# Kernel tuning notes

Hardware: AMD Instinct MI355X
Metric: run time of the kernel (lower is better)

The kernel has to match this reference:

```python
import jax, jax.numpy as jnp
import numpy as np

N_USERS = 100000
N_ITEMS = 50000
N_FACTORS = 64
N_LAYERS = 3
NNZ = 4800000


def setup_inputs() -> dict:
    key = jax.random.key(0)
    k1, k2, k3, k4, k5 = jax.random.split(key, 5)
    N = N_USERS + N_ITEMS
    return {
        "user_emb": 0.1 * jax.random.normal(k1, (N_USERS, N_FACTORS), dtype=jnp.float32),
        "item_emb": 0.1 * jax.random.normal(k2, (N_ITEMS, N_FACTORS), dtype=jnp.float32),
        "adj_row": jax.random.randint(k3, (NNZ,), 0, N, dtype=jnp.int32),
        "adj_col": jax.random.randint(k4, (NNZ,), 0, N, dtype=jnp.int32),
        "adj_val": jax.random.uniform(k5, (NNZ,), dtype=jnp.float32),
    }


def reference(user_emb, item_emb, adj_row, adj_col, adj_val):
    n_users = user_emb.shape[0]
    n_items = item_emb.shape[0]
    N = n_users + n_items

    # initial embeddings: concat users then items  [N, d]
    emb = jnp.concatenate([user_emb, item_emb], axis=0)

    def spmm(x):
        # sparse (COO) @ dense: gather source rows, scale, scatter-add to dest rows
        msgs = adj_val[:, None] * x[adj_col]          # [nnz, d]
        return jax.ops.segment_sum(msgs, adj_row, num_segments=N)

    # running mean over layer outputs (fuses stack+mean; dropout=0, eval mode)
    acc = emb
    for _ in range(N_LAYERS):
        emb = spmm(emb)
        acc = acc + emb
    mean_emb = acc / (N_LAYERS + 1)

    return mean_emb[:n_users], mean_emb[n_users:]
```

## Files before the change

### kernel.cpp

```cpp
#include <hip/hip_runtime.h>

static constexpr int D        = 64;
static constexpr int N_LAYERS = 3;
static constexpr int SH2      = 8;
static constexpr int T1       = 4096;
static constexpr int CAP      = 8896;
static constexpr int NINIT    = 448;


__device__ inline unsigned pack_bf2(float a, float b) {
    unsigned ua = __float_as_uint(a); ua = (ua + 0x7FFFu + ((ua >> 16) & 1u)) >> 16;
    unsigned ub = __float_as_uint(b); ub = (ub + 0x7FFFu + ((ub >> 16) & 1u)) >> 16;
    return ua | (ub << 16);
}
__device__ inline float blo(unsigned u) { return __uint_as_float(u << 16); }
__device__ inline float bhi(unsigned u) { return __uint_as_float(u & 0xFFFF0000u); }

__global__ __launch_bounds__(256) void k_part1f(const int* __restrict__ row,
                                                const int* __restrict__ col,
                                                const float* __restrict__ val,
                                                int* __restrict__ gcnt,
                                                unsigned* __restrict__ g1,
                                                unsigned char* __restrict__ lr,
                                                int nnz, int NB2, int nInit,
                                                const float4* __restrict__ ue,
                                                const float4* __restrict__ ie,
                                                uint4* __restrict__ cur,
                                                int nUser8, int nTot8) {
    __shared__ unsigned       sg1[T1];
    __shared__ unsigned char  slr[T1];
    __shared__ unsigned short bbin[T1];
    __shared__ unsigned short perm[T1];
    __shared__ int hist[768];
    __shared__ int binstart[768];
    __shared__ int gcur[768];
    __shared__ int bincur[768];
    __shared__ int wtot[4];

    int tid = threadIdx.x;
    int bid = blockIdx.x;
    int tile;
    if (bid < 2 * nInit) {
        if (bid & 1) {
            int stride = nInit * 256;
            for (int i = (bid >> 1) * 256 + tid; i < nTot8; i += stride) {
                float4 f0, f1;
                if (i < nUser8) { f0 = ue[2 * i];              f1 = ue[2 * i + 1]; }
                else            { int j = i - nUser8; f0 = ie[2 * j]; f1 = ie[2 * j + 1]; }
                cur[i] = make_uint4(pack_bf2(f0.x, f0.y), pack_bf2(f0.z, f0.w),
                                    pack_bf2(f1.x, f1.y), pack_bf2(f1.z, f1.w));
            }
            return;
        }
        tile = bid >> 1;
    } else {
        tile = bid - nInit;
    }

    int base = tile * T1;
    int n    = nnz - base; if (n > T1) n = T1;

    for (int b = tid; b < NB2; b += 256) { hist[b] = 0; bincur[b] = 0; }
    __syncthreads();

    for (int i = tid; i < n; i += 256) {
        int e = base + i;
        int r = row[e];
        int q = (int)(val[e] * 16384.f + 0.5f);
        if (q > 16383) q = 16383;
        sg1[i]  = ((unsigned)col[e] << 14) | (unsigned)q;
        slr[i]  = (unsigned char)(r & ((1 << SH2) - 1));
        int b   = r >> SH2;
        bbin[i] = (unsigned short)b;
        atomicAdd(&hist[b], 1);
    }
    __syncthreads();

    int per = (NB2 + 255) / 256;
    int i0  = tid * per;
    int sum = 0;
    for (int k = 0; k < per; ++k) { int i = i0 + k; if (i < NB2) sum += hist[i]; }
    int inc = sum;
    #pragma unroll
    for (int o = 1; o < 64; o <<= 1) {
        int t = __shfl_up(inc, o);
        if ((tid & 63) >= o) inc += t;
    }
    if ((tid & 63) == 63) wtot[tid >> 6] = inc;
    __syncthreads();
    int wbase = 0;
    int w = tid >> 6;
    #pragma unroll
    for (int j = 0; j < 3; ++j) if (w > j) wbase += wtot[j];
    int run = wbase + inc - sum;
    for (int k = 0; k < per; ++k) {
        int i = i0 + k;
        if (i < NB2) { binstart[i] = run; run += hist[i]; }
    }
    __syncthreads();

    for (int b = tid; b < NB2; b += 256) {
        int c = hist[b];
        if (c) {
            int o = atomicAdd(&gcnt[b], c);
            int lim = CAP - c;
            if (o > lim) o = lim;
            gcur[b] = b * CAP + o;
        }
    }
    __syncthreads();

    for (int i = tid; i < n; i += 256) {
        int b = bbin[i];
        int rnk = binstart[b] + atomicAdd(&bincur[b], 1);
        perm[rnk] = (unsigned short)i;
    }
    __syncthreads();

    for (int j = tid; j < n; j += 256) {
        int i = perm[j];
        int b = bbin[i];
        int pos = gcur[b] + (j - binstart[b]);
        g1[pos] = sg1[i];
        lr[pos] = slr[i];
    }
}

__global__ __launch_bounds__(512) void k_part2(const int* __restrict__ gcnt,
                                               const unsigned* __restrict__ g1,
                                               const unsigned char* __restrict__ lr,
                                               unsigned* __restrict__ ecv,
                                               int2* __restrict__ rowptr2) {
    __shared__ int hist[256];
    __shared__ int cur[256];
    __shared__ int ssum[256];
    int b   = blockIdx.x;
    int tid = threadIdx.x;
    int lo  = b * CAP;
    int cnt = gcnt[b];
    if (cnt > CAP) cnt = CAP;

    if (tid < 256) hist[tid] = 0;
    __syncthreads();
    for (int i = tid; i < cnt; i += 512)
        atomicAdd(&hist[lr[lo + i]], 1);
    __syncthreads();

    if (tid < 256) ssum[tid] = hist[tid];
    __syncthreads();
    for (int off = 1; off < 256; off <<= 1) {
        int v = 0;
        if (tid < 256 && tid >= off) v = ssum[tid - off];
        __syncthreads();
        if (tid < 256) ssum[tid] += v;
        __syncthreads();
    }
    if (tid < 256) {
        int h    = hist[tid];
        int excl = ssum[tid] - h;
        cur[tid] = excl;
        rowptr2[(b << SH2) + tid] = make_int2(lo + excl, lo + excl + h);
    }
    __syncthreads();

    for (int i = tid; i < cnt; i += 512) {
        int r = lr[lo + i];
        int p = atomicAdd(&cur[r], 1);
        ecv[lo + p] = g1[lo + i];
    }
}

template <bool LAST>
__global__ void k_spmm_bf(const int2* __restrict__ rowptr2,
                          const unsigned* __restrict__ ecv,
                          const uint4* __restrict__ x, uint4* __restrict__ y,
                          float* __restrict__ acc,
                          const uint4* __restrict__ e0b,
                          const uint4* __restrict__ y1,
                          int N) {
    int wid = (blockIdx.x * blockDim.x + threadIdx.x) >> 6;
    if (wid >= N) return;
    int lane = threadIdx.x & 63;
    int grp  = lane >> 3;
    unsigned ch = (unsigned)(lane & 7);
    int2 rp = rowptr2[wid];
    int e0 = rp.x;
    int e1 = rp.y;
    float s0 = 0.f, s1 = 0.f, s2 = 0.f, s3 = 0.f;
    float s4 = 0.f, s5 = 0.f, s6 = 0.f, s7 = 0.f;
    int e = e0 + grp;
    for (; e + 24 < e1; e += 32) {
        unsigned A0 = ecv[e];
        unsigned A1 = ecv[e + 8];
        unsigned A2 = ecv[e + 16];
        unsigned A3 = ecv[e + 24];
        uint4 x0 = x[((A0 >> 11) & ~7u) | ch];
        uint4 x1 = x[((A1 >> 11) & ~7u) | ch];
        uint4 x2 = x[((A2 >> 11) & ~7u) | ch];
        uint4 x3 = x[((A3 >> 11) & ~7u) | ch];
        float v0 = (float)(A0 & 0x3FFFu);
        float v1 = (float)(A1 & 0x3FFFu);
        float v2 = (float)(A2 & 0x3FFFu);
        float v3 = (float)(A3 & 0x3FFFu);
        s0 += v0 * blo(x0.x) + v1 * blo(x1.x) + v2 * blo(x2.x) + v3 * blo(x3.x);
        s1 += v0 * bhi(x0.x) + v1 * bhi(x1.x) + v2 * bhi(x2.x) + v3 * bhi(x3.x);
        s2 += v0 * blo(x0.y) + v1 * blo(x1.y) + v2 * blo(x2.y) + v3 * blo(x3.y);
        s3 += v0 * bhi(x0.y) + v1 * bhi(x1.y) + v2 * bhi(x2.y) + v3 * bhi(x3.y);
        s4 += v0 * blo(x0.z) + v1 * blo(x1.z) + v2 * blo(x2.z) + v3 * blo(x3.z);
        s5 += v0 * bhi(x0.z) + v1 * bhi(x1.z) + v2 * bhi(x2.z) + v3 * bhi(x3.z);
        s6 += v0 * blo(x0.w) + v1 * blo(x1.w) + v2 * blo(x2.w) + v3 * blo(x3.w);
        s7 += v0 * bhi(x0.w) + v1 * bhi(x1.w) + v2 * bhi(x2.w) + v3 * bhi(x3.w);
    }
    for (; e + 8 < e1; e += 16) {
        unsigned A = ecv[e];
        unsigned C = ecv[e + 8];
        uint4 xa = x[((A >> 11) & ~7u) | ch];
        uint4 xc = x[((C >> 11) & ~7u) | ch];
        float va = (float)(A & 0x3FFFu);
        float vc = (float)(C & 0x3FFFu);
        s0 += va * blo(xa.x) + vc * blo(xc.x);
        s1 += va * bhi(xa.x) + vc * bhi(xc.x);
        s2 += va * blo(xa.y) + vc * blo(xc.y);
        s3 += va * bhi(xa.y) + vc * bhi(xc.y);
        s4 += va * blo(xa.z) + vc * blo(xc.z);
        s5 += va * bhi(xa.z) + vc * bhi(xc.z);
        s6 += va * blo(xa.w) + vc * blo(xc.w);
        s7 += va * bhi(xa.w) + vc * bhi(xc.w);
    }
    if (e < e1) {
        unsigned A = ecv[e];
        uint4 xa = x[((A >> 11) & ~7u) | ch];
        float va = (float)(A & 0x3FFFu);
        s0 += va * blo(xa.x); s1 += va * bhi(xa.x);
        s2 += va * blo(xa.y); s3 += va * bhi(xa.y);
        s4 += va * blo(xa.z); s5 += va * bhi(xa.z);
        s6 += va * blo(xa.w); s7 += va * bhi(xa.w);
    }
    #pragma unroll
    for (int m = 8; m <= 32; m <<= 1) {
        s0 += __shfl_xor(s0, m); s1 += __shfl_xor(s1, m);
        s2 += __shfl_xor(s2, m); s3 += __shfl_xor(s3, m);
        s4 += __shfl_xor(s4, m); s5 += __shfl_xor(s5, m);
        s6 += __shfl_xor(s6, m); s7 += __shfl_xor(s7, m);
    }
    if (grp == 0) {
        if (!LAST) {
            const float SC = 1.f / 16384.f;
            y[(size_t)wid * 8 + ch] =
                make_uint4(pack_bf2(s0 * SC, s1 * SC), pack_bf2(s2 * SC, s3 * SC),
                           pack_bf2(s4 * SC, s5 * SC), pack_bf2(s6 * SC, s7 * SC));
        } else {
            const float SC25 = 0.25f / 16384.f;
            size_t ro = (size_t)wid * 8 + ch;
            uint4 u0 = e0b[ro];
            uint4 u1 = y1[ro];
            uint4 u2 = x [ro];
            float4 a0, a1;
            a0.x = (blo(u0.x) + blo(u1.x) + blo(u2.x)) * 0.25f + s0 * SC25;
            a0.y = (bhi(u0.x) + bhi(u1.x) + bhi(u2.x)) * 0.25f + s1 * SC25;
            a0.z = (blo(u0.y) + blo(u1.y) + blo(u2.y)) * 0.25f + s2 * SC25;
            a0.w = (bhi(u0.y) + bhi(u1.y) + bhi(u2.y)) * 0.25f + s3 * SC25;
            a1.x = (blo(u0.z) + blo(u1.z) + blo(u2.z)) * 0.25f + s4 * SC25;
            a1.y = (bhi(u0.z) + bhi(u1.z) + bhi(u2.z)) * 0.25f + s5 * SC25;
            a1.z = (blo(u0.w) + blo(u1.w) + blo(u2.w)) * 0.25f + s6 * SC25;
            a1.w = (bhi(u0.w) + bhi(u1.w) + bhi(u2.w)) * 0.25f + s7 * SC25;
            size_t o = ((size_t)wid << 6) + (ch << 3);
            *(float4*)(acc + o)     = a0;
            *(float4*)(acc + o + 4) = a1;
        }
    }
}

__global__ void k_init(const float4* __restrict__ ue, const float4* __restrict__ ie,
                       float4* __restrict__ cur, float4* __restrict__ acc,
                       int nUser4, int nTot4) {
    int stride = gridDim.x * blockDim.x;
    for (int i = blockIdx.x * blockDim.x + threadIdx.x; i < nTot4; i += stride) {
        float4 v = (i < nUser4) ? ue[i] : ie[i - nUser4];
        cur[i] = v;
        acc[i] = v;
    }
}

__global__ void k_spmm_atomic(const int* __restrict__ row, const int* __restrict__ col,
                              const float* __restrict__ val, const float* __restrict__ x,
                              float* __restrict__ y, int nnz) {
    long long total  = (long long)nnz * 16;
    long long stride = (long long)gridDim.x * blockDim.x;
    for (long long idx = (long long)blockIdx.x * blockDim.x + threadIdx.x;
         idx < total; idx += stride) {
        int e = (int)(idx >> 4);
        int c = (int)(idx & 15);
        int r = row[e];
        int ssrc = col[e];
        float v = val[e];
        float4 xv = *(const float4*)(x + (size_t)ssrc * D + c * 4);
        float* yp = y + (size_t)r * D + c * 4;
        atomicAdd(yp + 0, v * xv.x);
        atomicAdd(yp + 1, v * xv.y);
        atomicAdd(yp + 2, v * xv.z);
        atomicAdd(yp + 3, v * xv.w);
    }
}

__global__ void k_acc(const float4* __restrict__ nxt, float4* __restrict__ acc,
                      float scale, int n4) {
    int stride = gridDim.x * blockDim.x;
    for (int i = blockIdx.x * blockDim.x + threadIdx.x; i < n4; i += stride) {
        float4 a = acc[i];
        float4 b = nxt[i];
        a.x = (a.x + b.x) * scale;
        a.y = (a.y + b.y) * scale;
        a.z = (a.z + b.z) * scale;
        a.w = (a.w + b.w) * scale;
        acc[i] = a;
    }
}

extern "C" void kernel_launch(void* const* d_in, const int* in_sizes, int n_in,
                              void* d_out, int out_size, void* d_ws, size_t ws_size,
                              hipStream_t stream) {
    const float* ue  = (const float*)d_in[0];
    const float* ie  = (const float*)d_in[1];
    const int*   row = (const int*)  d_in[2];
    const int*   col = (const int*)  d_in[3];
    const float* val = (const float*)d_in[4];

    const int n_users = in_sizes[0] / D;
    const int n_items = in_sizes[1] / D;
    const int nnz     = in_sizes[2];
    const int N       = n_users + n_items;
    const int NB2     = (N + (1 << SH2) - 1) >> SH2;

    float* acc = (float*)d_out;
    const size_t bf16B = (size_t)N * D * 2;
    auto aup = [](size_t x) { return (x + 255) & ~(size_t)255; };

    size_t off = 0;
    uint4* buf0 = (uint4*)((char*)d_ws + off); off += aup(bf16B);
    uint4* buf1 = (uint4*)((char*)d_ws + off); off += aup(bf16B);
    uint4* buf2 = (uint4*)((char*)d_ws + off); off += aup(bf16B);
    unsigned*      g1 = (unsigned*)     ((char*)d_ws + off); off += aup((size_t)NB2 * CAP * 4);
    unsigned char* lr = (unsigned char*)((char*)d_ws + off); off += aup((size_t)NB2 * CAP);
    unsigned*      ecv = (unsigned*)    ((char*)d_ws + off); off += aup((size_t)NB2 * CAP * 4);
    int2* rowptr2 = (int2*)((char*)d_ws + off); off += aup((size_t)(NB2 << SH2) * 8);
    int*  gcnt    = (int*) ((char*)d_ws + off); off += aup((size_t)NB2 * 4);
    const size_t needCSR = off;

    bool capOK = ((size_t)nnz / NB2 + 600) <= (size_t)CAP && NB2 <= 768 &&
                 N <= (1 << 18);

    if (ws_size >= needCSR && capOK) {
        hipMemsetAsync(gcnt, 0, (size_t)NB2 * 4, stream);
        int nTiles = (nnz + T1 - 1) / T1;
        int nInit  = NINIT < nTiles ? NINIT : nTiles;
        int nTot8  = N * 8;
        int nUser8 = n_users * 8;
        k_part1f<<<nTiles + nInit, 256, 0, stream>>>(row, col, val, gcnt, g1, lr,
                                                     nnz, NB2, nInit,
                                                     (const float4*)ue, (const float4*)ie,
                                                     buf0, nUser8, nTot8);
        k_part2<<<NB2, 512, 0, stream>>>(gcnt, g1, lr, ecv, rowptr2);

        int grid = (N + 3) / 4;
        k_spmm_bf<false><<<grid, 256, 0, stream>>>(rowptr2, ecv, buf0, buf1,
                                                   nullptr, nullptr, nullptr, N);
        k_spmm_bf<false><<<grid, 256, 0, stream>>>(rowptr2, ecv, buf1, buf2,
                                                   nullptr, nullptr, nullptr, N);
        k_spmm_bf<true ><<<grid, 256, 0, stream>>>(rowptr2, ecv, buf2, nullptr,
                                                   acc, buf0, buf1, N);
    } else {
        const size_t denseB = (size_t)N * D * sizeof(float);
        float* fa = (float*)d_ws;
        float* fb = fa + (size_t)N * D;
        const int nTot4  = N * D / 4;
        const int nUser4 = n_users * D / 4;
        k_init<<<2048, 256, 0, stream>>>((const float4*)ue, (const float4*)ie,
                                         (float4*)fa, (float4*)acc, nUser4, nTot4);
        float* curp = fa;
        float* nxt  = fb;
        for (int l = 0; l < N_LAYERS; ++l) {
            hipMemsetAsync(nxt, 0, denseB, stream);
            k_spmm_atomic<<<8192, 256, 0, stream>>>(row, col, val, curp, nxt, nnz);
            float scale = (l == N_LAYERS - 1) ? (1.0f / (N_LAYERS + 1)) : 1.0f;
            k_acc<<<2048, 256, 0, stream>>>((const float4*)nxt, (float4*)acc, scale, nTot4);
            float* t = curp; curp = nxt; nxt = t;
        }
    }
}
```

Baseline: 470.5 us.

## Split CSR bucket build into histogram kernel and 4-way scatter kernel

The per-bucket CSR build kernel is split in two. The first computes row histograms and prefix offsets and writes per-row cursors to global memory. The second scatters edges using global atomics on those cursors, with four blocks per bucket. This raises parallelism beyond NB2 (~586) blocks, at the cost of an extra launch, global atomics instead of shared-memory ones, and a second read of lr.

```diff
diff --git a/kernel.cpp b/kernel.cpp
--- a/kernel.cpp
+++ b/kernel.cpp
@@ -126,13 +126,11 @@
     }
 }
 
-__global__ __launch_bounds__(512) void k_part2(const int* __restrict__ gcnt,
-                                               const unsigned* __restrict__ g1,
-                                               const unsigned char* __restrict__ lr,
-                                               unsigned* __restrict__ ecv,
-                                               int2* __restrict__ rowptr2) {
+__global__ __launch_bounds__(256) void k_part2a(const int* __restrict__ gcnt,
+                                                const unsigned char* __restrict__ lr,
+                                                int2* __restrict__ rowptr2,
+                                                int* __restrict__ grcur) {
     __shared__ int hist[256];
-    __shared__ int cur[256];
     __shared__ int ssum[256];
     int b   = blockIdx.x;
     int tid = threadIdx.x;
@@ -140,33 +138,42 @@
     int cnt = gcnt[b];
     if (cnt > CAP) cnt = CAP;
 
-    if (tid < 256) hist[tid] = 0;
-    __syncthreads();
-    for (int i = tid; i < cnt; i += 512)
+    hist[tid] = 0;
+    __syncthreads();
+    for (int i = tid; i < cnt; i += 256)
         atomicAdd(&hist[lr[lo + i]], 1);
     __syncthreads();
 
-    if (tid < 256) ssum[tid] = hist[tid];
+    int h = hist[tid];
+    ssum[tid] = h;
     __syncthreads();
     for (int off = 1; off < 256; off <<= 1) {
-        int v = 0;
-        if (tid < 256 && tid >= off) v = ssum[tid - off];
+        int v = (tid >= off) ? ssum[tid - off] : 0;
         __syncthreads();
-        if (tid < 256) ssum[tid] += v;
+        ssum[tid] += v;
         __syncthreads();
     }
-    if (tid < 256) {
-        int h    = hist[tid];
-        int excl = ssum[tid] - h;
-        cur[tid] = excl;
-        rowptr2[(b << SH2) + tid] = make_int2(lo + excl, lo + excl + h);
-    }
-    __syncthreads();
-
-    for (int i = tid; i < cnt; i += 512) {
+    int excl = ssum[tid] - h;
+    rowptr2[(b << SH2) + tid] = make_int2(lo + excl, lo + excl + h);
+    grcur  [(b << SH2) + tid] = lo + excl;
+}
+
+__global__ __launch_bounds__(256) void k_part2b(const int* __restrict__ gcnt,
+                                                const unsigned* __restrict__ g1,
+                                                const unsigned char* __restrict__ lr,
+                                                unsigned* __restrict__ ecv,
+                                                int* __restrict__ grcur) {
+    int b   = blockIdx.x >> 2;
+    int q   = blockIdx.x & 3;
+    int lo  = b * CAP;
+    int cnt = gcnt[b];
+    if (cnt > CAP) cnt = CAP;
+    int c0 = (cnt * q) >> 2;
+    int c1 = (cnt * (q + 1)) >> 2;
+    for (int i = c0 + threadIdx.x; i < c1; i += 256) {
         int r = lr[lo + i];
-        int p = atomicAdd(&cur[r], 1);
-        ecv[lo + p] = g1[lo + i];
+        int p = atomicAdd(&grcur[(b << SH2) + r], 1);
+        ecv[p] = g1[lo + i];
     }
 }
 
@@ -344,6 +351,7 @@
     unsigned char* lr = (unsigned char*)((char*)d_ws + off); off += aup((size_t)NB2 * CAP);
     unsigned*      ecv = (unsigned*)    ((char*)d_ws + off); off += aup((size_t)NB2 * CAP * 4);
     int2* rowptr2 = (int2*)((char*)d_ws + off); off += aup((size_t)(NB2 << SH2) * 8);
+    int*  grcur   = (int*) ((char*)d_ws + off); off += aup((size_t)(NB2 << SH2) * 4);
     int*  gcnt    = (int*) ((char*)d_ws + off); off += aup((size_t)NB2 * 4);
     const size_t needCSR = off;
 
@@ -360,7 +368,8 @@
                                                      nnz, NB2, nInit,
                                                      (const float4*)ue, (const float4*)ie,
                                                      buf0, nUser8, nTot8);
-        k_part2<<<NB2, 512, 0, stream>>>(gcnt, g1, lr, ecv, rowptr2);
+        k_part2a<<<NB2, 256, 0, stream>>>(gcnt, lr, rowptr2, grcur);
+        k_part2b<<<NB2 * 4, 256, 0, stream>>>(gcnt, g1, lr, ecv, grcur);
 
         int grid = (N + 3) / 4;
         k_spmm_bf<false><<<grid, 256, 0, stream>>>(rowptr2, ecv, buf0, buf1,
```

After: 545.6 us. +16.0%, slower.
